# Kernel tuning notes

Measured on AMD Instinct MI355X. Metric: run time of the kernel, lower is better.

The kernel has to match this reference:

```python
import jax, jax.numpy as jnp
import numpy as np

B, L, D = 32, 512, 256
MAX_DUR = 8


def setup_inputs() -> dict:
    key = jax.random.key(0)
    k1, k2 = jax.random.split(key)
    hidden_phonems = jax.random.normal(k1, (B, L, D), dtype=jnp.float32)
    durations = jax.random.randint(k2, (B, L), 0, MAX_DUR, dtype=jnp.int32)
    return {"hidden_phonems": hidden_phonems, "durations": durations}


def reference(hidden_phonems, durations):
    # hidden_phonems: [B, L, D], durations: [B, L] int
    totals = jnp.sum(durations, axis=1)                    # [B] mel length per utterance
    max_T = int(jnp.max(totals))                           # batch-max padded length (matches torch)
    cum = jnp.cumsum(durations, axis=1)                    # [B, L] exclusive-of-next prefix sums
    t = jnp.arange(max_T, dtype=jnp.int32)                 # output frame positions
    # frame t belongs to the first phoneme whose cumulative duration exceeds t
    idx = jax.vmap(lambda c: jnp.searchsorted(c, t, side='right'))(cum)  # [B, max_T]
    idx = jnp.clip(idx, 0, hidden_phonems.shape[1] - 1)
    out = jnp.take_along_axis(hidden_phonems, idx[:, :, None], axis=1)   # [B, max_T, D]
    mask = (t[None, :] < totals[:, None])                  # zero out padding frames
    return out * mask[:, :, None].astype(out.dtype)
```

## Files before the change

### kernel.cpp

```cpp
#include <hip/hip_runtime.h>
#include <hip/hip_bf16.h>

#define B_SZ 32
#define L_SZ 512
#define D_SZ 256
#define PHON_PER_WAVE 2
#define PHON_BLOCKS (B_SZ * L_SZ / (4 * PHON_PER_WAVE))
#define CUM_STRIDE 520
#define WS_NEEDED (B_SZ * CUM_STRIDE * 4)

typedef float  f4 __attribute__((ext_vector_type(4)));
typedef int    i4 __attribute__((ext_vector_type(4)));

__global__ void __launch_bounds__(512)
scan_kernel(const int* __restrict__ durations, int* __restrict__ cum) {
    const int lane = threadIdx.x & 63;
    const int wv   = threadIdx.x >> 6;
    const int b    = blockIdx.x * 8 + wv;

    const i4* drow = (const i4*)(durations + b * L_SZ);
    const i4 a = drow[lane * 2];
    const i4 c = drow[lane * 2 + 1];

    const int s1 = a.x;
    const int s2 = s1 + a.y;
    const int s3 = s2 + a.z;
    const int s4 = s3 + a.w;
    const int s5 = s4 + c.x;
    const int s6 = s5 + c.y;
    const int s7 = s6 + c.z;
    const int s8 = s7 + c.w;

    int ex = s8;
    #pragma unroll
    for (int off = 1; off < 64; off <<= 1) {
        const int t = __shfl_up(ex, off, 64);
        if (lane >= off) ex += t;
    }
    ex -= s8;

    i4* crow = (i4*)(cum + b * CUM_STRIDE);
    i4 o1, o2;
    o1.x = ex + s1; o1.y = ex + s2; o1.z = ex + s3; o1.w = ex + s4;
    o2.x = ex + s5; o2.y = ex + s6; o2.z = ex + s7; o2.w = ex + s8;
    crow[lane * 2]     = o1;
    crow[lane * 2 + 1] = o2;
}

__global__ void __launch_bounds__(256)
lr_copy_kernel(const float* __restrict__ hidden,
               const int* __restrict__ cum,
               float* __restrict__ out,
               int maxT) {
    const int tid  = threadIdx.x;
    const int lane = tid & 63;
    const int wave = tid >> 6;

    const int wid = blockIdx.x * 4 + wave;
    const int b   = wid >> 8;
    const int w   = wid & 255;
    const int l0  = w * 2;

    const f4* src0 = (const f4*)(hidden + ((size_t)(b * L_SZ + l0)) * D_SZ);
    const f4 v0 = __builtin_nontemporal_load(src0 + lane);
    const f4 v1 = __builtin_nontemporal_load(src0 + lane + 64);

    const int* crow = cum + b * CUM_STRIDE;
    const int start0 = (l0 == 0) ? 0 : crow[l0 - 1];
    const int c0     = crow[l0];
    const int c1     = crow[l0 + 1];
    const int total  = crow[511];

    const int d0     = c0 - start0;
    const int start1 = c0;
    const int d1     = c1 - c0;

    f4* dst0 = (f4*)(out + ((size_t)b * maxT + start0) * D_SZ) + lane;
    f4* dst1 = (f4*)(out + ((size_t)b * maxT + start1) * D_SZ) + lane;
    #pragma unroll
    for (int j = 0; j < 7; ++j) {
        if (j < d0) __builtin_nontemporal_store(v0, dst0 + j * 64);
        if (j < d1) __builtin_nontemporal_store(v1, dst1 + j * 64);
    }

    const f4 z = (f4){0.f, 0.f, 0.f, 0.f};
    for (int t = total + w; t < maxT; t += 256) {
        f4* dst = (f4*)(out + ((size_t)b * maxT + t) * D_SZ);
        __builtin_nontemporal_store(z, dst + lane);
    }
}

__global__ void __launch_bounds__(256)
lr_kernel(const float* __restrict__ hidden,
          const int* __restrict__ durations,
          float* __restrict__ out,
          int maxT) {
    const int tid  = threadIdx.x;
    const int lane = tid & 63;
    const int wave = tid >> 6;

    const int wid = blockIdx.x * 4 + wave;
    const int b   = wid >> 8;
    const int w   = wid & 255;
    const int l0  = w * 2;

    const f4* src0 = (const f4*)(hidden + ((size_t)(b * L_SZ + l0)) * D_SZ);
    const f4 v0 = __builtin_nontemporal_load(src0 + lane);
    const f4 v1 = __builtin_nontemporal_load(src0 + lane + 64);

    const i4* drow = (const i4*)(durations + b * L_SZ);
    const i4 a = drow[lane * 2];
    const i4 c = drow[lane * 2 + 1];

    const int base = lane * 8;
    int p = 0;
    p += ((base + 0 < l0) ? a.x : 0) + (a.x << 16);
    p += ((base + 1 < l0) ? a.y : 0) + (a.y << 16);
    p += ((base + 2 < l0) ? a.z : 0) + (a.z << 16);
    p += ((base + 3 < l0) ? a.w : 0) + (a.w << 16);
    p += ((base + 4 < l0) ? c.x : 0) + (c.x << 16);
    p += ((base + 5 < l0) ? c.y : 0) + (c.y << 16);
    p += ((base + 6 < l0) ? c.z : 0) + (c.z << 16);
    p += ((base + 7 < l0) ? c.w : 0) + (c.w << 16);
    #pragma unroll
    for (int off = 32; off; off >>= 1) p += __shfl_xor(p, off, 64);
    const int start0 = p & 0xffff;
    const int total  = ((unsigned)p) >> 16;

    const int k = l0 & 7;
    const int p0 = (k < 4) ? (k == 0 ? a.x : a.z) : (k == 4 ? c.x : c.z);
    const int p1 = (k < 4) ? (k == 0 ? a.y : a.w) : (k == 4 ? c.y : c.w);
    const int d0 = __shfl(p0, l0 >> 3, 64);
    const int d1 = __shfl(p1, l0 >> 3, 64);
    const int start1 = start0 + d0;

    f4* dst0 = (f4*)(out + ((size_t)b * maxT + start0) * D_SZ) + lane;
    f4* dst1 = (f4*)(out + ((size_t)b * maxT + start1) * D_SZ) + lane;
    #pragma unroll
    for (int j = 0; j < 7; ++j) {
        if (j < d0) __builtin_nontemporal_store(v0, dst0 + j * 64);
        if (j < d1) __builtin_nontemporal_store(v1, dst1 + j * 64);
    }

    const f4 z = (f4){0.f, 0.f, 0.f, 0.f};
    for (int t = total + w; t < maxT; t += 256) {
        f4* dst = (f4*)(out + ((size_t)b * maxT + t) * D_SZ);
        __builtin_nontemporal_store(z, dst + lane);
    }
}

extern "C" void kernel_launch(void* const* d_in, const int* in_sizes, int n_in,
                              void* d_out, int out_size, void* d_ws, size_t ws_size,
                              hipStream_t stream) {
    const float* hidden = (const float*)d_in[0];
    const int* durations = (const int*)d_in[1];
    float* out = (float*)d_out;

    const int maxT = out_size / (B_SZ * D_SZ);

    if (ws_size >= (size_t)WS_NEEDED && d_ws != nullptr) {
        int* cum = (int*)d_ws;
        scan_kernel<<<4, 512, 0, stream>>>(durations, cum);
        lr_copy_kernel<<<PHON_BLOCKS, 256, 0, stream>>>(hidden, cum, out, maxT);
    } else {
        lr_kernel<<<PHON_BLOCKS, 256, 0, stream>>>(hidden, durations, out, maxT);
    }
}
```

Measured before the change: 87.93 us.

## Fuse scan into single kernel with 8 phonemes per wave and packed durations

Drops the separate scan kernel and workspace path, so one kernel computes each wave's start offset with a per-lane row sum and a wave reduction. Each wave now handles 8 consecutive phonemes, reading the 8 durations from one 3-bit-packed shuffle and writing all their frames in order. Output stores switch from nontemporal to regular stores. This removes a kernel launch and the dependency on the cumulative buffer, at the cost of fewer waves, more registers per wave, and packing that assumes durations below 8.

```diff
diff --git a/kernel.cpp b/kernel.cpp
--- a/kernel.cpp
+++ b/kernel.cpp
@@ -1,151 +1,62 @@
 #include <hip/hip_runtime.h>
-#include <hip/hip_bf16.h>
 
 #define B_SZ 32
 #define L_SZ 512
 #define D_SZ 256
-#define PHON_PER_WAVE 2
-#define PHON_BLOCKS (B_SZ * L_SZ / (4 * PHON_PER_WAVE))
-#define CUM_STRIDE 520
-#define WS_NEEDED (B_SZ * CUM_STRIDE * 4)
+#define P_PER_WAVE 8
+#define WAVES_TOTAL (B_SZ * L_SZ / P_PER_WAVE)
+#define BLOCKS (WAVES_TOTAL / 4)
 
-typedef float  f4 __attribute__((ext_vector_type(4)));
-typedef int    i4 __attribute__((ext_vector_type(4)));
-
-__global__ void __launch_bounds__(512)
-scan_kernel(const int* __restrict__ durations, int* __restrict__ cum) {
-    const int lane = threadIdx.x & 63;
-    const int wv   = threadIdx.x >> 6;
-    const int b    = blockIdx.x * 8 + wv;
-
-    const i4* drow = (const i4*)(durations + b * L_SZ);
-    const i4 a = drow[lane * 2];
-    const i4 c = drow[lane * 2 + 1];
-
-    const int s1 = a.x;
-    const int s2 = s1 + a.y;
-    const int s3 = s2 + a.z;
-    const int s4 = s3 + a.w;
-    const int s5 = s4 + c.x;
-    const int s6 = s5 + c.y;
-    const int s7 = s6 + c.z;
-    const int s8 = s7 + c.w;
-
-    int ex = s8;
-    #pragma unroll
-    for (int off = 1; off < 64; off <<= 1) {
-        const int t = __shfl_up(ex, off, 64);
-        if (lane >= off) ex += t;
-    }
-    ex -= s8;
-
-    i4* crow = (i4*)(cum + b * CUM_STRIDE);
-    i4 o1, o2;
-    o1.x = ex + s1; o1.y = ex + s2; o1.z = ex + s3; o1.w = ex + s4;
-    o2.x = ex + s5; o2.y = ex + s6; o2.z = ex + s7; o2.w = ex + s8;
-    crow[lane * 2]     = o1;
-    crow[lane * 2 + 1] = o2;
-}
-
-__global__ void __launch_bounds__(256)
-lr_copy_kernel(const float* __restrict__ hidden,
-               const int* __restrict__ cum,
-               float* __restrict__ out,
-               int maxT) {
-    const int tid  = threadIdx.x;
-    const int lane = tid & 63;
-    const int wave = tid >> 6;
-
-    const int wid = blockIdx.x * 4 + wave;
-    const int b   = wid >> 8;
-    const int w   = wid & 255;
-    const int l0  = w * 2;
-
-    const f4* src0 = (const f4*)(hidden + ((size_t)(b * L_SZ + l0)) * D_SZ);
-    const f4 v0 = __builtin_nontemporal_load(src0 + lane);
-    const f4 v1 = __builtin_nontemporal_load(src0 + lane + 64);
-
-    const int* crow = cum + b * CUM_STRIDE;
-    const int start0 = (l0 == 0) ? 0 : crow[l0 - 1];
-    const int c0     = crow[l0];
-    const int c1     = crow[l0 + 1];
-    const int total  = crow[511];
-
-    const int d0     = c0 - start0;
-    const int start1 = c0;
-    const int d1     = c1 - c0;
-
-    f4* dst0 = (f4*)(out + ((size_t)b * maxT + start0) * D_SZ) + lane;
-    f4* dst1 = (f4*)(out + ((size_t)b * maxT + start1) * D_SZ) + lane;
-    #pragma unroll
-    for (int j = 0; j < 7; ++j) {
-        if (j < d0) __builtin_nontemporal_store(v0, dst0 + j * 64);
-        if (j < d1) __builtin_nontemporal_store(v1, dst1 + j * 64);
-    }
-
-    const f4 z = (f4){0.f, 0.f, 0.f, 0.f};
-    for (int t = total + w; t < maxT; t += 256) {
-        f4* dst = (f4*)(out + ((size_t)b * maxT + t) * D_SZ);
-        __builtin_nontemporal_store(z, dst + lane);
-    }
-}
+typedef float f4 __attribute__((ext_vector_type(4)));
+typedef int   i4 __attribute__((ext_vector_type(4)));
 
 __global__ void __launch_bounds__(256)
 lr_kernel(const float* __restrict__ hidden,
           const int* __restrict__ durations,
           float* __restrict__ out,
           int maxT) {
-    const int tid  = threadIdx.x;
-    const int lane = tid & 63;
-    const int wave = tid >> 6;
+    const int lane = threadIdx.x & 63;
+    const int wv   = threadIdx.x >> 6;
+    const int wid  = blockIdx.x * 4 + wv;
+    const int b    = wid >> 6;
+    const int g    = wid & 63;
+    const int l0   = g * P_PER_WAVE;
 
-    const int wid = blockIdx.x * 4 + wave;
-    const int b   = wid >> 8;
-    const int w   = wid & 255;
-    const int l0  = w * 2;
-
-    const f4* src0 = (const f4*)(hidden + ((size_t)(b * L_SZ + l0)) * D_SZ);
-    const f4 v0 = __builtin_nontemporal_load(src0 + lane);
-    const f4 v1 = __builtin_nontemporal_load(src0 + lane + 64);
+    const f4* src = (const f4*)(hidden + ((size_t)(b * L_SZ + l0)) * D_SZ) + lane;
+    f4 v[8];
+    #pragma unroll
+    for (int r = 0; r < 8; ++r) v[r] = __builtin_nontemporal_load(src + r * 64);
 
     const i4* drow = (const i4*)(durations + b * L_SZ);
     const i4 a = drow[lane * 2];
     const i4 c = drow[lane * 2 + 1];
+    const int s = a.x + a.y + a.z + a.w + c.x + c.y + c.z + c.w;
+    const int packed = a.x | (a.y << 3) | (a.z << 6) | (a.w << 9)
+                     | (c.x << 12) | (c.y << 15) | (c.z << 18) | (c.w << 21);
 
-    const int base = lane * 8;
-    int p = 0;
-    p += ((base + 0 < l0) ? a.x : 0) + (a.x << 16);
-    p += ((base + 1 < l0) ? a.y : 0) + (a.y << 16);
-    p += ((base + 2 < l0) ? a.z : 0) + (a.z << 16);
-    p += ((base + 3 < l0) ? a.w : 0) + (a.w << 16);
-    p += ((base + 4 < l0) ? c.x : 0) + (c.x << 16);
-    p += ((base + 5 < l0) ? c.y : 0) + (c.y << 16);
-    p += ((base + 6 < l0) ? c.z : 0) + (c.z << 16);
-    p += ((base + 7 < l0) ? c.w : 0) + (c.w << 16);
+    int p = ((lane < g) ? s : 0) + (s << 16);
     #pragma unroll
     for (int off = 32; off; off >>= 1) p += __shfl_xor(p, off, 64);
-    const int start0 = p & 0xffff;
-    const int total  = ((unsigned)p) >> 16;
+    int start       = p & 0xffff;
+    const int total = ((unsigned)p) >> 16;
 
-    const int k = l0 & 7;
-    const int p0 = (k < 4) ? (k == 0 ? a.x : a.z) : (k == 4 ? c.x : c.z);
-    const int p1 = (k < 4) ? (k == 0 ? a.y : a.w) : (k == 4 ? c.y : c.w);
-    const int d0 = __shfl(p0, l0 >> 3, 64);
-    const int d1 = __shfl(p1, l0 >> 3, 64);
-    const int start1 = start0 + d0;
+    const int pk = __shfl(packed, g, 64);
 
-    f4* dst0 = (f4*)(out + ((size_t)b * maxT + start0) * D_SZ) + lane;
-    f4* dst1 = (f4*)(out + ((size_t)b * maxT + start1) * D_SZ) + lane;
+    float* obase = out + (size_t)b * maxT * D_SZ;
     #pragma unroll
-    for (int j = 0; j < 7; ++j) {
-        if (j < d0) __builtin_nontemporal_store(v0, dst0 + j * 64);
-        if (j < d1) __builtin_nontemporal_store(v1, dst1 + j * 64);
+    for (int r = 0; r < 8; ++r) {
+        const int d = (pk >> (3 * r)) & 7;
+        f4* dst = (f4*)(obase + (size_t)start * D_SZ) + lane;
+        #pragma unroll
+        for (int j = 0; j < 7; ++j)
+            if (j < d) dst[j * 64] = v[r];
+        start += d;
     }
 
     const f4 z = (f4){0.f, 0.f, 0.f, 0.f};
-    for (int t = total + w; t < maxT; t += 256) {
-        f4* dst = (f4*)(out + ((size_t)b * maxT + t) * D_SZ);
-        __builtin_nontemporal_store(z, dst + lane);
+    for (int t = total + g; t < maxT; t += 64) {
+        f4* dst = (f4*)(obase + (size_t)t * D_SZ) + lane;
+        *dst = z;
     }
 }
 
@@ -158,11 +69,5 @@
 
     const int maxT = out_size / (B_SZ * D_SZ);
 
-    if (ws_size >= (size_t)WS_NEEDED && d_ws != nullptr) {
-        int* cum = (int*)d_ws;
-        scan_kernel<<<4, 512, 0, stream>>>(durations, cum);
-        lr_copy_kernel<<<PHON_BLOCKS, 256, 0, stream>>>(hidden, cum, out, maxT);
-    } else {
-        lr_kernel<<<PHON_BLOCKS, 256, 0, stream>>>(hidden, durations, out, maxT);
-    }
+    lr_kernel<<<BLOCKS, 256, 0, stream>>>(hidden, durations, out, maxT);
 }
```

Result: faster. 83.78 us (-4.7%).
